# Kernel tuning notes

Hardware: AMD Instinct MI355X
Metric: run time of the kernel (lower is better)

## Reference

```python
import jax, jax.numpy as jnp
import numpy as np


def _batch_conv2d(inputs, kernels):
    # inputs: [B, 1, H, W], kernels: [B, 1, 3, 3]; distinct kernel per sample
    # Implemented as a grouped conv: view inputs as [1, B, H, W], groups=B.
    B, _, H, W = inputs.shape
    out = jax.lax.conv_general_dilated(
        inputs.reshape(1, B, H, W),
        kernels,  # OIHW with O=B, I=1
        window_strides=(1, 1),
        padding=((1, 1), (1, 1)),
        feature_group_count=B,
        dimension_numbers=("NCHW", "OIHW", "NCHW"),
    )
    return out.reshape(B, 1, H, W)


def setup_inputs() -> dict:
    key = jax.random.key(0)
    k1, k2, k3 = jax.random.split(key, 3)
    B, m = 64, 512
    x = jax.random.normal(k1, (B, 1, m, m), dtype=jnp.float32)
    f = jax.random.normal(k2, (B, 1, m, m), dtype=jnp.float32)
    kernelA = jax.random.normal(k3, (B, 1, 3, 3), dtype=jnp.float32)
    return {"x": x, "f": f, "kernelA": kernelA}


def reference(x, f, kernelA):
    # One Jacobi-style smoothing step: x <- x + (f - A x) / 6
    Ax = _batch_conv2d(x, kernelA)
    x = x + (f - Ax) * (1.0 / 6.0)
    return x
```

## Files before the change

kernel.cpp:

```cpp
#include <hip/hip_runtime.h>

#define BB 64
#define HH 512
#define WW 512
#define RPT 2
#define ROWS_PER_BLOCK (4 * RPT)
#define NBLOCKS (BB * HH / ROWS_PER_BLOCK)

struct Row { float4 v0, v1; float l, r; };

__device__ __forceinline__ void accum(float4& q0, float4& q1, const Row& w,
                                      float w0, float w1, float w2) {
    q0.x += w0 * w.l    + w1 * w.v0.x + w2 * w.v0.y;
    q0.y += w0 * w.v0.x + w1 * w.v0.y + w2 * w.v0.z;
    q0.z += w0 * w.v0.y + w1 * w.v0.z + w2 * w.v0.w;
    q0.w += w0 * w.v0.z + w1 * w.v0.w + w2 * w.v1.x;
    q1.x += w0 * w.v0.w + w1 * w.v1.x + w2 * w.v1.y;
    q1.y += w0 * w.v1.x + w1 * w.v1.y + w2 * w.v1.z;
    q1.z += w0 * w.v1.y + w1 * w.v1.z + w2 * w.v1.w;
    q1.w += w0 * w.v1.z + w1 * w.v1.w + w2 * w.r;
}

__global__ __launch_bounds__(256) void jacobi_v7_kernel(
    const float* __restrict__ x,
    const float* __restrict__ f,
    const float* __restrict__ k,
    float* __restrict__ out)
{
    const int tid  = threadIdx.x;
    const int lane = tid & 63;
    const int wv   = tid >> 6;

    const int b  = blockIdx.x >> 6;
    const int rb = blockIdx.x & 63;
    const int r0 = (rb << 3) + wv * RPT;

    const size_t img = (size_t)b * (HH * WW);
    const float* xb = x + img;
    const float* fb = f + img;
    float*       ob = out + img;

    const float* kb = k + b * 9;
    const float k00 = kb[0], k01 = kb[1], k02 = kb[2];
    const float k10 = kb[3], k11 = kb[4], k12 = kb[5];
    const float k20 = kb[6], k21 = kb[7], k22 = kb[8];

    const int col = lane << 3;

    Row rows[RPT + 2];
    #pragma unroll
    for (int t = 0; t < RPT + 2; ++t) {
        const int rr = r0 - 1 + t;
        if (rr >= 0 && rr < HH) {
            const float* p = xb + (size_t)rr * WW + col;
            rows[t].v0 = *(const float4*)p;
            rows[t].v1 = *(const float4*)(p + 4);
        } else {
            rows[t].v0 = make_float4(0.f, 0.f, 0.f, 0.f);
            rows[t].v1 = make_float4(0.f, 0.f, 0.f, 0.f);
        }
    }

    #pragma unroll
    for (int t = 0; t < RPT + 2; ++t) {
        const float lh = __shfl_up(rows[t].v1.w, 1);
        const float rh = __shfl_down(rows[t].v0.x, 1);
        rows[t].l = (lane == 0)  ? 0.f : lh;
        rows[t].r = (lane == 63) ? 0.f : rh;
    }

    const float inv6 = 1.f / 6.f;
    #pragma unroll
    for (int r = 0; r < RPT; ++r) {
        const size_t off = (size_t)(r0 + r) * WW + col;
        const float4 f0 = *(const float4*)(fb + off);
        const float4 f1 = *(const float4*)(fb + off + 4);

        float4 q0 = make_float4(0.f, 0.f, 0.f, 0.f);
        float4 q1 = make_float4(0.f, 0.f, 0.f, 0.f);
        accum(q0, q1, rows[r],     k00, k01, k02);
        accum(q0, q1, rows[r + 1], k10, k11, k12);
        accum(q0, q1, rows[r + 2], k20, k21, k22);

        const Row& c = rows[r + 1];
        float4 o0, o1;
        o0.x = c.v0.x + (f0.x - q0.x) * inv6;
        o0.y = c.v0.y + (f0.y - q0.y) * inv6;
        o0.z = c.v0.z + (f0.z - q0.z) * inv6;
        o0.w = c.v0.w + (f0.w - q0.w) * inv6;
        o1.x = c.v1.x + (f1.x - q1.x) * inv6;
        o1.y = c.v1.y + (f1.y - q1.y) * inv6;
        o1.z = c.v1.z + (f1.z - q1.z) * inv6;
        o1.w = c.v1.w + (f1.w - q1.w) * inv6;

        *(float4*)(ob + off)     = o0;
        *(float4*)(ob + off + 4) = o1;
    }
}

extern "C" void kernel_launch(void* const* d_in, const int* in_sizes, int n_in,
                              void* d_out, int out_size, void* d_ws, size_t ws_size,
                              hipStream_t stream) {
    const float* x  = (const float*)d_in[0];
    const float* f  = (const float*)d_in[1];
    const float* kk = (const float*)d_in[2];
    float* out = (float*)d_out;

    jacobi_v7_kernel<<<NBLOCKS, 256, 0, stream>>>(x, f, kk, out);
}
```

Before: 174.8 us.

## Split each lane's 8 columns into two coalesced half-row float4 chunks and hoist f loads

Each lane now handles columns [4*lane, 4*lane+4) and [256+4*lane, ...) instead of 8 contiguous columns, so every wave-wide float4 load and store covers a fully contiguous 1 KB segment rather than a strided pattern. Halo values at the half-row seam are passed with extra cross-lane shuffles from lane 63 and lane 0. The f loads are moved ahead of the compute and fenced with a sched_barrier so all global loads are issued together. This is meant to improve coalescing and memory-level parallelism, at the cost of a few more shuffles per row and higher register pressure.

```diff
diff --git a/kernel.cpp b/kernel.cpp
--- a/kernel.cpp
+++ b/kernel.cpp
@@ -7,21 +7,17 @@
 #define ROWS_PER_BLOCK (4 * RPT)
 #define NBLOCKS (BB * HH / ROWS_PER_BLOCK)
 
-struct Row { float4 v0, v1; float l, r; };
+struct Q { float4 v; float l, r; };
 
-__device__ __forceinline__ void accum(float4& q0, float4& q1, const Row& w,
-                                      float w0, float w1, float w2) {
-    q0.x += w0 * w.l    + w1 * w.v0.x + w2 * w.v0.y;
-    q0.y += w0 * w.v0.x + w1 * w.v0.y + w2 * w.v0.z;
-    q0.z += w0 * w.v0.y + w1 * w.v0.z + w2 * w.v0.w;
-    q0.w += w0 * w.v0.z + w1 * w.v0.w + w2 * w.v1.x;
-    q1.x += w0 * w.v0.w + w1 * w.v1.x + w2 * w.v1.y;
-    q1.y += w0 * w.v1.x + w1 * w.v1.y + w2 * w.v1.z;
-    q1.z += w0 * w.v1.y + w1 * w.v1.z + w2 * w.v1.w;
-    q1.w += w0 * w.v1.z + w1 * w.v1.w + w2 * w.r;
+__device__ __forceinline__ void accumq(float4& q, const Q& w,
+                                       float w0, float w1, float w2) {
+    q.x += w0 * w.l   + w1 * w.v.x + w2 * w.v.y;
+    q.y += w0 * w.v.x + w1 * w.v.y + w2 * w.v.z;
+    q.z += w0 * w.v.y + w1 * w.v.z + w2 * w.v.w;
+    q.w += w0 * w.v.z + w1 * w.v.w + w2 * w.r;
 }
 
-__global__ __launch_bounds__(256) void jacobi_v7_kernel(
+__global__ __launch_bounds__(256) void jacobi_v8_kernel(
     const float* __restrict__ x,
     const float* __restrict__ f,
     const float* __restrict__ k,
@@ -45,56 +41,74 @@
     const float k10 = kb[3], k11 = kb[4], k12 = kb[5];
     const float k20 = kb[6], k21 = kb[7], k22 = kb[8];
 
-    const int col = lane << 3;
+    const int col = lane << 2;
 
-    Row rows[RPT + 2];
+    float4 xa[RPT + 2], xq[RPT + 2];
     #pragma unroll
     for (int t = 0; t < RPT + 2; ++t) {
         const int rr = r0 - 1 + t;
         if (rr >= 0 && rr < HH) {
             const float* p = xb + (size_t)rr * WW + col;
-            rows[t].v0 = *(const float4*)p;
-            rows[t].v1 = *(const float4*)(p + 4);
+            xa[t] = *(const float4*)p;
+            xq[t] = *(const float4*)(p + 256);
         } else {
-            rows[t].v0 = make_float4(0.f, 0.f, 0.f, 0.f);
-            rows[t].v1 = make_float4(0.f, 0.f, 0.f, 0.f);
+            xa[t] = make_float4(0.f, 0.f, 0.f, 0.f);
+            xq[t] = make_float4(0.f, 0.f, 0.f, 0.f);
         }
     }
+    float4 fa[RPT], fq[RPT];
+    #pragma unroll
+    for (int r = 0; r < RPT; ++r) {
+        const float* p = fb + (size_t)(r0 + r) * WW + col;
+        fa[r] = *(const float4*)p;
+        fq[r] = *(const float4*)(p + 256);
+    }
+    __builtin_amdgcn_sched_barrier(0);
 
+    Q A[RPT + 2], B[RPT + 2];
     #pragma unroll
     for (int t = 0; t < RPT + 2; ++t) {
-        const float lh = __shfl_up(rows[t].v1.w, 1);
-        const float rh = __shfl_down(rows[t].v0.x, 1);
-        rows[t].l = (lane == 0)  ? 0.f : lh;
-        rows[t].r = (lane == 63) ? 0.f : rh;
+        const float a_l  = __shfl_up(xa[t].w, 1);
+        const float a_r  = __shfl_down(xa[t].x, 1);
+        const float b_l  = __shfl_up(xq[t].w, 1);
+        const float b_r  = __shfl_down(xq[t].x, 1);
+        const float aw63 = __shfl(xa[t].w, 63);
+        const float bx0  = __shfl(xq[t].x, 0);
+        A[t].v = xa[t];
+        B[t].v = xq[t];
+        A[t].l = (lane == 0)  ? 0.f  : a_l;
+        A[t].r = (lane == 63) ? bx0  : a_r;
+        B[t].l = (lane == 0)  ? aw63 : b_l;
+        B[t].r = (lane == 63) ? 0.f  : b_r;
     }
 
     const float inv6 = 1.f / 6.f;
     #pragma unroll
     for (int r = 0; r < RPT; ++r) {
-        const size_t off = (size_t)(r0 + r) * WW + col;
-        const float4 f0 = *(const float4*)(fb + off);
-        const float4 f1 = *(const float4*)(fb + off + 4);
+        float4 qa = make_float4(0.f, 0.f, 0.f, 0.f);
+        float4 qb = make_float4(0.f, 0.f, 0.f, 0.f);
+        accumq(qa, A[r],     k00, k01, k02);
+        accumq(qa, A[r + 1], k10, k11, k12);
+        accumq(qa, A[r + 2], k20, k21, k22);
+        accumq(qb, B[r],     k00, k01, k02);
+        accumq(qb, B[r + 1], k10, k11, k12);
+        accumq(qb, B[r + 2], k20, k21, k22);
 
-        float4 q0 = make_float4(0.f, 0.f, 0.f, 0.f);
-        float4 q1 = make_float4(0.f, 0.f, 0.f, 0.f);
-        accum(q0, q1, rows[r],     k00, k01, k02);
-        accum(q0, q1, rows[r + 1], k10, k11, k12);
-        accum(q0, q1, rows[r + 2], k20, k21, k22);
+        const float4 ca = A[r + 1].v;
+        const float4 cb = B[r + 1].v;
+        float4 oa, obq;
+        oa.x  = ca.x + (fa[r].x - qa.x) * inv6;
+        oa.y  = ca.y + (fa[r].y - qa.y) * inv6;
+        oa.z  = ca.z + (fa[r].z - qa.z) * inv6;
+        oa.w  = ca.w + (fa[r].w - qa.w) * inv6;
+        obq.x = cb.x + (fq[r].x - qb.x) * inv6;
+        obq.y = cb.y + (fq[r].y - qb.y) * inv6;
+        obq.z = cb.z + (fq[r].z - qb.z) * inv6;
+        obq.w = cb.w + (fq[r].w - qb.w) * inv6;
 
-        const Row& c = rows[r + 1];
-        float4 o0, o1;
-        o0.x = c.v0.x + (f0.x - q0.x) * inv6;
-        o0.y = c.v0.y + (f0.y - q0.y) * inv6;
-        o0.z = c.v0.z + (f0.z - q0.z) * inv6;
-        o0.w = c.v0.w + (f0.w - q0.w) * inv6;
-        o1.x = c.v1.x + (f1.x - q1.x) * inv6;
-        o1.y = c.v1.y + (f1.y - q1.y) * inv6;
-        o1.z = c.v1.z + (f1.z - q1.z) * inv6;
-        o1.w = c.v1.w + (f1.w - q1.w) * inv6;
-
-        *(float4*)(ob + off)     = o0;
-        *(float4*)(ob + off + 4) = o1;
+        float* po = ob + (size_t)(r0 + r) * WW + col;
+        *(float4*)po         = oa;
+        *(float4*)(po + 256) = obq;
     }
 }
 
@@ -106,5 +120,5 @@
     const float* kk = (const float*)d_in[2];
     float* out = (float*)d_out;
 
-    jacobi_v7_kernel<<<NBLOCKS, 256, 0, stream>>>(x, f, kk, out);
+    jacobi_v8_kernel<<<NBLOCKS, 256, 0, stream>>>(x, f, kk, out);
 }
```

Result: faster. 170.5 us (-2.5%).
